# Kernel optimization log

Measured on AMD Instinct MI355X. Metric: run time of the kernel, lower is better.

## Reference

```python
import jax, jax.numpy as jnp
import numpy as np

B, T, D = 2, 4096, 1024
HD, HQ, KVH, W = 128, 8, 1, 1024   # head_dim, q_heads, kv_heads, window
HH, HG, K = 1536, 2048, 4          # hawk hidden, gmlp hidden, conv kernel
ALPHA_SCALE = float(np.log(8.0))   # alpha_log_scale (stored as log, used exp'd)


def setup_inputs() -> dict:
    key = jax.random.key(0)
    ks = jax.random.split(key, 16)
    n = lambda k, shape, std: jax.random.normal(k, shape, jnp.float32) * std
    return {
        'x': n(ks[0], (B, T, D), 1.0),
        'sn_g': jnp.ones((D,), jnp.float32),
        'q_w': n(ks[1], (HQ * HD, D), D ** -0.5),
        'kv_w': n(ks[2], (2 * KVH * HD, D), D ** -0.5),
        'ao_w': n(ks[3], (D, D), D ** -0.5),
        'sgn_g': jnp.ones((D,), jnp.float32),
        'sg_grow': n(ks[4], (2 * HG, D), D ** -0.5),
        'sg_shrink': n(ks[5], (D, HG), HG ** -0.5),
        'hn_g': jnp.ones((D,), jnp.float32),
        'h_in_w': n(ks[6], (2 * HH, D), D ** -0.5),
        'h_conv_w': n(ks[7], (HH, 1, K), K ** -0.5),
        'h_conv_b': jnp.zeros((HH,), jnp.float32),
        'h_gates_w': n(ks[8], (2 * HH, HH), HH ** -0.5),
        'h_gates_b': jnp.zeros((2 * HH,), jnp.float32),
        'h_forget': jnp.linspace(-4.323, -9.0, HH, dtype=jnp.float32),
        'h_out_w': n(ks[9], (D, HH), HH ** -0.5),
        'hgn_g': jnp.ones((D,), jnp.float32),
        'hg_grow': n(ks[10], (2 * HG, D), D ** -0.5),
        'hg_shrink': n(ks[11], (D, HG), HG ** -0.5),
    }


def rmsnorm(x, gamma):
    # original: gamma / dim**-0.5 * x / ||x||_2  (no eps)
    inv = jax.lax.rsqrt(jnp.sum(x * x, axis=-1, keepdims=True))
    return gamma * (x.shape[-1] ** 0.5) * x * inv


def rope(x, base=10000.0):
    # x: (B, T, H, HD); interleaved rotary over time axis 1
    t = x.shape[1]
    hd = x.shape[-1]
    inv = 1.0 / (base ** (jnp.arange(0, hd, 2, dtype=jnp.float32) / hd))
    ang = jnp.arange(t, dtype=jnp.float32)[:, None] * inv[None, :]  # (T, HD/2)
    cos = jnp.cos(ang)[None, :, None, :]
    sin = jnp.sin(ang)[None, :, None, :]
    x1, x2 = x[..., 0::2], x[..., 1::2]
    y1 = x1 * cos - x2 * sin
    y2 = x1 * sin + x2 * cos
    return jnp.stack([y1, y2], axis=-1).reshape(x.shape)


def sliding_mqa(x, q_w, kv_w, ao_w):
    # MQA with causal sliding window of W, computed in blocks of W
    q = (x @ q_w.T).reshape(B, T, HQ, HD)
    kv = (x @ kv_w.T).reshape(B, T, 2, KVH, HD)
    k = kv[:, :, 0, 0]  # (B, T, HD) since KVH == 1
    v = kv[:, :, 1, 0]
    q = rope(q)
    k = rope(k[:, :, None, :])[:, :, 0]
    nb = T // W
    qb = q.reshape(B, nb, W, HQ, HD)
    kb = k.reshape(B, nb, W, HD)
    vb = v.reshape(B, nb, W, HD)
    # prepend previous block (zeros for block 0)
    shift = lambda a: jnp.concatenate([jnp.zeros_like(a[:, :1]), a[:, :-1]], axis=1)
    k2 = jnp.concatenate([shift(kb), kb], axis=2)  # (B, nb, 2W, HD)
    v2 = jnp.concatenate([shift(vb), vb], axis=2)
    qi = jnp.arange(W)[:, None]
    kj = jnp.arange(2 * W)[None, :]
    base = (kj >= qi) & (kj <= qi + W)  # causal + window (i-j <= W)
    blk0 = base & (kj >= W)             # block 0 has no real previous block
    mask = jnp.where(jnp.arange(nb)[:, None, None] == 0, blk0[None], base[None])
    scores = jnp.einsum('bnqhd,bnkd->bhnqk', qb, k2) * (HD ** -0.5)
    scores = jnp.where(mask[None, None], scores, -jnp.inf)
    p = jax.nn.softmax(scores, axis=-1)
    o = jnp.einsum('bhnqk,bnkd->bnqhd', p, v2).reshape(B, T, HQ * HD)
    return o @ ao_w.T


def gated_mlp(x, grow_w, shrink_w):
    gate, h = jnp.split(x @ grow_w.T, 2, axis=-1)
    return (jax.nn.gelu(gate, approximate=False) * h) @ shrink_w.T


def hawk(x, in_w, conv_w, conv_b, gates_w, gates_b, forget_base, out_w):
    gate, u = jnp.split(x @ in_w.T, 2, axis=-1)  # (B, T, HH) each
    # depthwise causal conv1d (torch pads k-1 both sides then slices [:T])
    u_nch = jnp.transpose(u, (0, 2, 1))  # (B, HH, T)
    c = jax.lax.conv_general_dilated(
        u_nch, conv_w, window_strides=(1,), padding=[(K - 1, 0)],
        feature_group_count=HH, dimension_numbers=('NCH', 'OIH', 'NCH'))
    xc = jnp.transpose(c + conv_b[None, :, None], (0, 2, 1))  # (B, T, HH)
    fg, ig = jnp.split(xc @ gates_w.T + gates_b, 2, axis=-1)
    log_alpha = -np.exp(ALPHA_SCALE) * jax.nn.softplus(forget_base) * jax.nn.sigmoid(fg)
    alpha = jnp.exp(log_alpha)
    beta = jnp.sqrt(1.0 - alpha * alpha + 1e-6)
    xin = beta * jax.nn.sigmoid(ig) * xc
    # linear recurrence h_t = alpha_t * h_{t-1} + xin_t  via associative scan
    def combine(c1, c2):
        a1, x1 = c1
        a2, x2 = c2
        return a1 * a2, a2 * x1 + x2
    _, h = jax.lax.associative_scan(combine, (alpha, xin), axis=1)
    return (jax.nn.gelu(gate, approximate=False) * h) @ out_w.T


def reference(x, sn_g, q_w, kv_w, ao_w, sgn_g, sg_grow, sg_shrink,
              hn_g, h_in_w, h_conv_w, h_conv_b, h_gates_w, h_gates_b,
              h_forget, h_out_w, hgn_g, hg_grow, hg_shrink):
    x = x + sliding_mqa(rmsnorm(x, sn_g), q_w, kv_w, ao_w)
    x = x + gated_mlp(rmsnorm(x, sgn_g), sg_grow, sg_shrink)
    x = x + hawk(rmsnorm(x, hn_g), h_in_w, h_conv_w, h_conv_b,
                 h_gates_w, h_gates_b, h_forget, h_out_w)
    x = x + gated_mlp(rmsnorm(x, hgn_g), hg_grow, hg_shrink)
    return x
```

## Files before the change

### kernel.cpp

```cpp
#include <hip/hip_runtime.h>
#include <hip/hip_bf16.h>
#include <math.h>

#define B_  2
#define T_  4096
#define D_  1024
#define HD_ 128
#define HQ_ 8
#define W_  1024
#define HH_ 1536
#define HG_ 2048
#define KC_ 4

typedef float  f32x4  __attribute__((ext_vector_type(4)));
typedef float  f32x2  __attribute__((ext_vector_type(2)));
typedef __bf16 bf16x8 __attribute__((ext_vector_type(8)));
typedef unsigned short u16;
typedef unsigned short u16x2 __attribute__((ext_vector_type(2)));
typedef unsigned short u16x4 __attribute__((ext_vector_type(4)));
typedef unsigned short u16x8 __attribute__((ext_vector_type(8)));

__device__ __forceinline__ u16 f2bf(float f) {
    unsigned int u = __builtin_bit_cast(unsigned int, f);
    u += 0x7fffu + ((u >> 16) & 1u);
    return (u16)(u >> 16);
}
__device__ __forceinline__ float bf2f(u16 v) {
    unsigned int u = ((unsigned int)v) << 16;
    return __builtin_bit_cast(float, u);
}
__device__ __forceinline__ float gelu_exact(float x) {
    return 0.5f * x * (1.0f + erff(x * 0.70710678118654752f));
}
__device__ __forceinline__ float sigmoidf_(float x) {
    return 1.0f / (1.0f + expf(-x));
}

#define GLOAD16(gp, lp) __builtin_amdgcn_global_load_lds( \
    (const __attribute__((address_space(1))) void*)(gp),  \
    (__attribute__((address_space(3))) void*)(lp), 16, 0, 0)

struct CvtArgs {
    const float* src[10];
    u16* dst[10];
    long cum[11];
};
__global__ __launch_bounds__(256)
void cvt_all_kernel(CvtArgs a)
{
    long i = ((long)blockIdx.x * 256 + threadIdx.x) * 8;
    if (i >= a.cum[10]) return;
    int seg = 0;
#pragma unroll
    for (int s = 1; s < 10; s++) if (i >= a.cum[s]) seg = s;
    long off = i - a.cum[seg];
    const float* src = a.src[seg];
    u16* dst = a.dst[seg];
    f32x4 x = *(const f32x4*)(src + off);
    f32x4 y = *(const f32x4*)(src + off + 4);
    u16x4 ua, ub;
    ua.x = f2bf(x.x); ua.y = f2bf(x.y); ua.z = f2bf(x.z); ua.w = f2bf(x.w);
    ub.x = f2bf(y.x); ub.y = f2bf(y.y); ub.z = f2bf(y.z); ub.w = f2bf(y.w);
    *(u16x4*)(dst + off) = ua;
    *(u16x4*)(dst + off + 4) = ub;
}

template<int EPI, bool OBF>
__global__ __launch_bounds__(512)
void gemm_big_kernel(const u16* __restrict__ A, const u16* __restrict__ Bw,
                     const float* __restrict__ bias, const float* __restrict__ res,
                     const u16* gatebuf, void* outv,
                     int M, int N, int K)
{
    __shared__ u16 lA[3][256 * 32];
    __shared__ u16 lB[3][128 * 32];
    const int wg0 = blockIdx.x + gridDim.x * blockIdx.y;
    const int cpx = (gridDim.x * gridDim.y) >> 3;
    const int wgs = (wg0 & 7) * cpx + (wg0 >> 3);
    const int n0 = (wgs % gridDim.x) * 128, m0 = (wgs / gridDim.x) * 256;
    const int tid = threadIdx.x, w = tid >> 6, l = tid & 63;
    const int wr = w >> 1, wc = w & 1;
    const int lr = l & 15, lg = l >> 4;

    f32x4 acc[4][4];
#pragma unroll
    for (int i = 0; i < 4; i++)
#pragma unroll
        for (int j = 0; j < 4; j++) acc[i][j] = {0.f, 0.f, 0.f, 0.f};

    const int srow = tid >> 2;
    const int gslot = (((tid) & 3) - ((tid >> 3) & 3)) & 3;
    const u16* gA = A + (long)(m0 + srow) * K + gslot * 8;
    const u16* gB = Bw + (long)(n0 + srow) * K + gslot * 8;
    const int lofs = tid * 8;

#define STAGE_G(buf, kk)                                            \
    {                                                               \
        GLOAD16(gA + (kk),                 &lA[buf][lofs]);         \
        GLOAD16(gA + (long)128 * K + (kk), &lA[buf][4096 + lofs]);  \
        GLOAD16(gB + (kk),                 &lB[buf][lofs]);         \
    }

    const int NT = K >> 5;
    STAGE_G(0, 0);
    STAGE_G(1, 32);

    const int swzr = (lr >> 1) & 3;
    int cur = 0;
    for (int t = 0; t < NT; ++t) {
        if (t == NT - 1) { asm volatile("s_waitcnt vmcnt(0)" ::: "memory"); }
        else             { asm volatile("s_waitcnt vmcnt(3)" ::: "memory"); }
        __builtin_amdgcn_s_barrier();
        __builtin_amdgcn_sched_barrier(0);
        if (t + 2 < NT) {
            int nb = cur + 2; if (nb >= 3) nb -= 3;
            STAGE_G(nb, (t + 2) << 5);
        }
        bf16x8 af[4], bfr[4];
#pragma unroll
        for (int m = 0; m < 4; m++)
            af[m] = *(const bf16x8*)&lA[cur][(wr * 64 + m * 16 + lr) * 32 + (((lg + swzr) & 3) * 8)];
#pragma unroll
        for (int n = 0; n < 4; n++)
            bfr[n] = *(const bf16x8*)&lB[cur][(wc * 64 + n * 16 + lr) * 32 + (((lg + swzr) & 3) * 8)];
        __builtin_amdgcn_s_setprio(1);
#pragma unroll
        for (int m = 0; m < 4; m++)
#pragma unroll
            for (int n = 0; n < 4; n++)
                acc[m][n] = __builtin_amdgcn_mfma_f32_16x16x32_bf16(af[m], bfr[n], acc[m][n], 0, 0, 0);
        __builtin_amdgcn_s_setprio(0);
        cur++; if (cur == 3) cur = 0;
    }
#undef STAGE_G

#pragma unroll
    for (int m = 0; m < 4; m++)
#pragma unroll
        for (int n = 0; n < 4; n++) {
            const int col = n0 + wc * 64 + n * 16 + lr;
            const float bv = (EPI == 1) ? bias[col] : 0.f;
#pragma unroll
            for (int r = 0; r < 4; r++) {
                const int row = m0 + wr * 64 + m * 16 + lg * 4 + r;
                const long idx = (long)row * N + col;
                float v = acc[m][n][r] + bv;
                if (EPI == 2) v += res[idx];
                if (EPI == 3) v = gelu_exact(bf2f(gatebuf[idx])) * v;
                if (OBF) ((u16*)outv)[idx] = f2bf(v);
                else     ((float*)outv)[idx] = v;
            }
        }
}

template<int EPI, bool OBF>
__global__ __launch_bounds__(256)
void gemm_bf16_kernel(const u16* __restrict__ A, const u16* __restrict__ Bw,
                      const float* __restrict__ bias, const float* __restrict__ res,
                      const u16* gatebuf, void* outv,
                      int M, int N, int K)
{
    __shared__ u16 lA[3][128 * 32];
    __shared__ u16 lB[3][128 * 32];
    const int wg0 = blockIdx.x + gridDim.x * blockIdx.y;
    const int cpx = (gridDim.x * gridDim.y) >> 3;
    const int wgs = (wg0 & 7) * cpx + (wg0 >> 3);
    const int n0 = (wgs % gridDim.x) * 128, m0 = (wgs / gridDim.x) * 128;
    const int tid = threadIdx.x, w = tid >> 6, l = tid & 63;
    const int wr = w >> 1, wc = w & 1, lr = l & 15, lg = l >> 4;

    f32x4 acc[4][4];
#pragma unroll
    for (int i = 0; i < 4; i++)
#pragma unroll
        for (int j = 0; j < 4; j++) acc[i][j] = {0.f, 0.f, 0.f, 0.f};

    const int srow = w * 16 + (l >> 2);
    const int gslot = ((l & 3) - ((l >> 3) & 3)) & 3;
    const u16* gA = A + (long)(m0 + srow) * K + gslot * 8;
    const u16* gB = Bw + (long)(n0 + srow) * K + gslot * 8;
    const int lofs = w * 512 + l * 8;

#define STAGE_G(buf, kk)                                          \
    {                                                             \
        GLOAD16(gA + (kk),                &lA[buf][lofs]);        \
        GLOAD16(gA + (long)64 * K + (kk), &lA[buf][2048 + lofs]); \
        GLOAD16(gB + (kk),                &lB[buf][lofs]);        \
        GLOAD16(gB + (long)64 * K + (kk), &lB[buf][2048 + lofs]); \
    }

    const int NT = K >> 5;
    STAGE_G(0, 0);
    STAGE_G(1, 32);

    const int swzr = (lr >> 1) & 3;
    int cur = 0;
    for (int t = 0; t < NT; ++t) {
        if (t == NT - 1) { asm volatile("s_waitcnt vmcnt(0)" ::: "memory"); }
        else             { asm volatile("s_waitcnt vmcnt(4)" ::: "memory"); }
        __builtin_amdgcn_s_barrier();
        __builtin_amdgcn_sched_barrier(0);
        if (t + 2 < NT) {
            int nb = cur + 2; if (nb >= 3) nb -= 3;
            STAGE_G(nb, (t + 2) << 5);
        }
        bf16x8 af[4], bfr[4];
#pragma unroll
        for (int m = 0; m < 4; m++)
            af[m] = *(const bf16x8*)&lA[cur][(wr * 64 + m * 16 + lr) * 32 + (((lg + swzr) & 3) * 8)];
#pragma unroll
        for (int n = 0; n < 4; n++)
            bfr[n] = *(const bf16x8*)&lB[cur][(wc * 64 + n * 16 + lr) * 32 + (((lg + swzr) & 3) * 8)];
        __builtin_amdgcn_s_setprio(1);
#pragma unroll
        for (int m = 0; m < 4; m++)
#pragma unroll
            for (int n = 0; n < 4; n++)
                acc[m][n] = __builtin_amdgcn_mfma_f32_16x16x32_bf16(af[m], bfr[n], acc[m][n], 0, 0, 0);
        __builtin_amdgcn_s_setprio(0);
        cur++; if (cur == 3) cur = 0;
    }
#undef STAGE_G

#pragma unroll
    for (int m = 0; m < 4; m++)
#pragma unroll
        for (int n = 0; n < 4; n++) {
            const int col = n0 + wc * 64 + n * 16 + lr;
            const float bv = (EPI == 1) ? bias[col] : 0.f;
#pragma unroll
            for (int r = 0; r < 4; r++) {
                const int row = m0 + wr * 64 + m * 16 + lg * 4 + r;
                const long idx = (long)row * N + col;
                float v = acc[m][n][r] + bv;
                if (EPI == 2) v += res[idx];
                if (EPI == 3) v = gelu_exact(bf2f(gatebuf[idx])) * v;
                if (OBF) ((u16*)outv)[idx] = f2bf(v);
                else     ((float*)outv)[idx] = v;
            }
        }
}

__global__ __launch_bounds__(256)
void rmsnorm_kernel(const float* __restrict__ x, const float* __restrict__ g,
                    u16* __restrict__ out)
{
    const long row = blockIdx.x;
    const int tid = threadIdx.x;
    const float* xp = x + row * D_;
    f32x4 v = *(const f32x4*)(xp + tid * 4);
    float ss = v.x * v.x + v.y * v.y + v.z * v.z + v.w * v.w;
#pragma unroll
    for (int o = 1; o < 64; o <<= 1) ss += __shfl_xor(ss, o);
    __shared__ float ps[4];
    if ((tid & 63) == 0) ps[tid >> 6] = ss;
    __syncthreads();
    float tot = ps[0] + ps[1] + ps[2] + ps[3];
    float inv = rsqrtf(tot) * 32.0f;
    f32x4 gv = *(const f32x4*)(g + tid * 4);
    u16x4 o4;
    o4.x = f2bf(gv.x * v.x * inv); o4.y = f2bf(gv.y * v.y * inv);
    o4.z = f2bf(gv.z * v.z * inv); o4.w = f2bf(gv.w * v.w * inv);
    *(u16x4*)(out + row * D_ + tid * 4) = o4;
}

__global__ void rope_bf16_kernel(const float* __restrict__ q, const float* __restrict__ kv,
                                 u16* __restrict__ qb, u16* __restrict__ kb)
{
    const long NQ = (long)B_ * T_ * HQ_ * 64;
    const long NK = (long)B_ * T_ * 64;
    long idx = (long)blockIdx.x * blockDim.x + threadIdx.x;
    if (idx >= NQ + NK) return;
    int i; long t; const float* src; u16* dst;
    if (idx < NQ) {
        i = idx & 63;
        long bth = idx >> 6;
        t = (bth / HQ_) % T_;
        src = q + bth * HD_ + 2 * i;
        dst = qb + bth * HD_ + 2 * i;
    } else {
        long k = idx - NQ;
        i = k & 63;
        long bt = k >> 6;
        t = bt % T_;
        src = kv + bt * (2 * HD_) + 2 * i;
        dst = kb + bt * HD_ + 2 * i;
    }
    float freq = exp2f(-(float)i * 0.20762050593046014f);
    float ang = (float)t * freq;
    float sn, cs;
    sincosf(ang, &sn, &cs);
    f32x2 xv = *(const f32x2*)src;
    u16x2 yv;
    yv.x = f2bf(xv.x * cs - xv.y * sn);
    yv.y = f2bf(xv.x * sn + xv.y * cs);
    *(u16x2*)dst = yv;
}

__global__ __launch_bounds__(256)
void vtrans_kernel(const float* __restrict__ kv, u16* __restrict__ vt)
{
    __shared__ float tile[64][65];
    const int t0 = blockIdx.x * 64, d0 = blockIdx.y * 64, b = blockIdx.z;
    const int tid = threadIdx.x;
    {
        const int tl = tid & 63, dg = tid >> 6;
        const float* vp = kv + (((long)b * T_ + t0 + tl) * 2 + 1) * HD_ + d0 + dg * 16;
#pragma unroll
        for (int j = 0; j < 4; j++) {
            f32x4 v = *(const f32x4*)(vp + j * 4);
            tile[dg * 16 + j * 4 + 0][tl] = v.x;
            tile[dg * 16 + j * 4 + 1][tl] = v.y;
            tile[dg * 16 + j * 4 + 2][tl] = v.z;
            tile[dg * 16 + j * 4 + 3][tl] = v.w;
        }
    }
    __syncthreads();
    {
        const int dl = tid >> 2, tg = (tid & 3) * 16;
        u16x8 a, c;
#pragma unroll
        for (int j = 0; j < 8; j++) a[j] = f2bf(tile[dl][tg + j]);
#pragma unroll
        for (int j = 0; j < 8; j++) c[j] = f2bf(tile[dl][tg + 8 + j]);
        u16* dst = vt + ((long)b * HD_ + d0 + dl) * T_ + t0 + tg;
        *(u16x8*)dst = a;
        *(u16x8*)(dst + 8) = c;
    }
}

#define PLD 72

__global__ __launch_bounds__(256)
void attn_mfma3_kernel(const u16* __restrict__ qb, const u16* __restrict__ kb,
                       const u16* __restrict__ vt, u16* __restrict__ o)
{
    __shared__ u16 Ksh[2][64 * 128];
    __shared__ u16 Vsh[2][128 * 64];
    __shared__ u16 Psh[4 * 16 * PLD];

    const int qt = blockIdx.x, h = blockIdx.y, b = blockIdx.z;
    const int q0 = qt * 64;
    const int tid = threadIdx.x;
    const int w = tid >> 6, l = tid & 63;
    const int lr = l & 15, lg = l >> 4;

    bf16x8 qfr[4];
    {
        const u16* qp = qb + (((long)b * T_ + q0 + w * 16 + lr) * HQ_ + h) * HD_;
#pragma unroll
        for (int kt = 0; kt < 4; kt++)
            qfr[kt] = *(const bf16x8*)(qp + kt * 32 + lg * 8);
    }

    int oK[4], oV[4];
#pragma unroll
    for (int i = 0; i < 4; i++) {
        int krow = w * 16 + i * 4 + (l >> 4);
        int kc8 = (l & 15) ^ (krow & 7);
        oK[i] = krow * 128 + kc8 * 8;
        int vrow = w * 32 + i * 8 + (l >> 3);
        int vc8 = (l & 7) ^ (vrow & 7);
        oV[i] = vrow * T_ + vc8 * 8;
    }
    const u16* kbase = kb + (long)b * T_ * HD_;
    const u16* vbase = vt + (long)b * HD_ * T_;

    f32x4 oacc[8];
#pragma unroll
    for (int dt = 0; dt < 8; dt++) oacc[dt] = {0.f, 0.f, 0.f, 0.f};
    float mrun[4], srun[4];
#pragma unroll
    for (int r = 0; r < 4; r++) { mrun[r] = -1e30f; srun[r] = 0.f; }

    const int kt_lo = (q0 >= W_) ? (q0 - W_) : 0;
    const int nt = ((q0 - kt_lo) >> 6) + 1;
    const int sw = lr & 7;
    const float scale = 0.08838834764831845f;

#pragma unroll
    for (int i = 0; i < 4; i++) {
        GLOAD16(kbase + (long)kt_lo * HD_ + oK[i], &Ksh[0][w * 2048 + i * 512]);
        GLOAD16(vbase + kt_lo + oV[i], &Vsh[0][w * 2048 + i * 512]);
    }

    for (int t = 0; t < nt; ++t) {
        const int kt0 = kt_lo + t * 64;
        const int cur = t & 1;
        if (t + 1 < nt) {
            const int ktn = kt0 + 64;
#pragma unroll
            for (int i = 0; i < 4; i++) {
                GLOAD16(kbase + (long)ktn * HD_ + oK[i], &Ksh[cur ^ 1][w * 2048 + i * 512]);
                GLOAD16(vbase + ktn + oV[i], &Vsh[cur ^ 1][w * 2048 + i * 512]);
            }
            asm volatile("s_waitcnt vmcnt(8)" ::: "memory");
        } else {
            asm volatile("s_waitcnt vmcnt(0)" ::: "memory");
        }
        __builtin_amdgcn_s_barrier();
        __builtin_amdgcn_sched_barrier(0);

        const u16* Kc = Ksh[cur];
        const u16* Vc = Vsh[cur];

        f32x4 s[4];
        __builtin_amdgcn_s_setprio(1);
#pragma unroll
        for (int ct = 0; ct < 4; ct++) {
            s[ct] = {0.f, 0.f, 0.f, 0.f};
#pragma unroll
            for (int kt = 0; kt < 4; kt++) {
                bf16x8 kf = *(const bf16x8*)&Kc[(ct * 16 + lr) * 128 + (((kt * 4 + lg) ^ sw) * 8)];
                s[ct] = __builtin_amdgcn_mfma_f32_16x16x32_bf16(qfr[kt], kf, s[ct], 0, 0, 0);
            }
        }
        __builtin_amdgcn_s_setprio(0);

        float tmax[4] = {-3e38f, -3e38f, -3e38f, -3e38f};
        if (kt0 == q0) {
#pragma unroll
            for (int ct = 0; ct < 4; ct++) {
                const int kpos = kt0 + ct * 16 + lr;
#pragma unroll
                for (int r = 0; r < 4; r++) {
                    const int qpos = q0 + w * 16 + lg * 4 + r;
                    float v = s[ct][r] * scale;
                    v = (kpos <= qpos) ? v : -3e38f;
                    s[ct][r] = v;
                    tmax[r] = fmaxf(tmax[r], v);
                }
            }
        } else if (kt0 == q0 - W_) {
#pragma unroll
            for (int ct = 0; ct < 4; ct++) {
                const int kpos = kt0 + ct * 16 + lr;
#pragma unroll
                for (int r = 0; r < 4; r++) {
                    const int qpos = q0 + w * 16 + lg * 4 + r;
                    float v = s[ct][r] * scale;
                    v = (kpos + W_ >= qpos) ? v : -3e38f;
                    s[ct][r] = v;
                    tmax[r] = fmaxf(tmax[r], v);
                }
            }
        } else {
#pragma unroll
            for (int ct = 0; ct < 4; ct++)
#pragma unroll
                for (int r = 0; r < 4; r++) {
                    float v = s[ct][r] * scale;
                    s[ct][r] = v;
                    tmax[r] = fmaxf(tmax[r], v);
                }
        }
#pragma unroll
        for (int r = 0; r < 4; r++)
#pragma unroll
            for (int msk = 1; msk < 16; msk <<= 1)
                tmax[r] = fmaxf(tmax[r], __shfl_xor(tmax[r], msk));

        bool defer = (tmax[0] <= mrun[0] + 8.f) && (tmax[1] <= mrun[1] + 8.f) &&
                     (tmax[2] <= mrun[2] + 8.f) && (tmax[3] <= mrun[3] + 8.f);
        if (!__all(defer)) {
            float frv[4];
#pragma unroll
            for (int r = 0; r < 4; r++) {
                float mnew = fmaxf(mrun[r], tmax[r]);
                frv[r] = __expf(mrun[r] - mnew);
                mrun[r] = mnew;
                srun[r] *= frv[r];
            }
#pragma unroll
            for (int dt = 0; dt < 8; dt++) {
                oacc[dt][0] *= frv[0]; oacc[dt][1] *= frv[1];
                oacc[dt][2] *= frv[2]; oacc[dt][3] *= frv[3];
            }
        }

        u16* pw = &Psh[w * 16 * PLD];
        float psum[4] = {0.f, 0.f, 0.f, 0.f};
#pragma unroll
        for (int ct = 0; ct < 4; ct++)
#pragma unroll
            for (int r = 0; r < 4; r++) {
                float p = __expf(s[ct][r] - mrun[r]);
                psum[r] += p;
                pw[(lg * 4 + r) * PLD + ct * 16 + lr] = f2bf(p);
            }
#pragma unroll
        for (int r = 0; r < 4; r++) {
#pragma unroll
            for (int msk = 1; msk < 16; msk <<= 1)
                psum[r] += __shfl_xor(psum[r], msk);
            srun[r] += psum[r];
        }

        asm volatile("s_waitcnt lgkmcnt(0)" ::: "memory");
        bf16x8 pa0 = *(const bf16x8*)&pw[lr * PLD + lg * 8];
        bf16x8 pa1 = *(const bf16x8*)&pw[lr * PLD + 32 + lg * 8];
        __builtin_amdgcn_s_setprio(1);
#pragma unroll
        for (int dt = 0; dt < 8; dt++) {
            bf16x8 vf0 = *(const bf16x8*)&Vc[(dt * 16 + lr) * 64 + ((lg ^ sw) * 8)];
            bf16x8 vf1 = *(const bf16x8*)&Vc[(dt * 16 + lr) * 64 + (((4 + lg) ^ sw) * 8)];
            oacc[dt] = __builtin_amdgcn_mfma_f32_16x16x32_bf16(pa0, vf0, oacc[dt], 0, 0, 0);
            oacc[dt] = __builtin_amdgcn_mfma_f32_16x16x32_bf16(pa1, vf1, oacc[dt], 0, 0, 0);
        }
        __builtin_amdgcn_s_setprio(0);
        __syncthreads();
    }

#pragma unroll
    for (int r = 0; r < 4; r++) {
        const int qpos = q0 + w * 16 + lg * 4 + r;
        float inv = 1.f / srun[r];
        u16* op = o + ((long)b * T_ + qpos) * (HQ_ * HD_) + h * HD_;
#pragma unroll
        for (int dt = 0; dt < 8; dt++)
            op[dt * 16 + lr] = f2bf(oacc[dt][r] * inv);
    }
}

__global__ void conv_kernel(const u16* __restrict__ u, const float* __restrict__ w,
                            const float* __restrict__ bias, u16* __restrict__ xc)
{
    long idx = (long)blockIdx.x * blockDim.x + threadIdx.x;
    if (idx >= (long)B_ * T_ * HH_) return;
    int ch = (int)(idx % HH_);
    long row = idx / HH_;
    int t = (int)(row % T_);
    float acc = bias[ch];
#pragma unroll
    for (int k = 0; k < KC_; k++) {
        int ts = t - 3 + k;
        if (ts >= 0) acc += bf2f(u[(row - t + ts) * HH_ + ch]) * w[ch * KC_ + k];
    }
    xc[idx] = f2bf(acc);
}

#define CS_ 64
#define NC_ (T_ / CS_)

__device__ __forceinline__ void alpha_xin(const u16 fg, const u16 ig, const u16 xc,
                                          float sp, float& a, float& xin)
{
    a = expf(-8.0f * sp * sigmoidf_(bf2f(fg)));
    xin = sqrtf(1.f - a * a + 1e-6f) * sigmoidf_(bf2f(ig)) * bf2f(xc);
}

__global__ void scan1_kernel(const u16* __restrict__ fg, const u16* __restrict__ ig,
                             const u16* __restrict__ xc, const float* __restrict__ fb,
                             float* __restrict__ P, float* __restrict__ L)
{
    long idx = (long)blockIdx.x * blockDim.x + threadIdx.x;
    if (idx >= (long)B_ * NC_ * HH_) return;
    int ch = (int)(idx % HH_);
    int chunk = (int)((idx / HH_) % NC_);
    int b = (int)(idx / ((long)HH_ * NC_));
    long base = ((long)b * T_ + chunk * CS_) * HH_ + ch;
    float f = fb[ch];
    float sp = (f > 20.f) ? f : log1pf(expf(f));
    float p = 1.f, lacc = 0.f;
    for (int i = 0; i < CS_; i++) {
        long o = base + (long)i * HH_;
        float a, xin;
        alpha_xin(fg[o], ig[o], xc[o], sp, a, xin);
        lacc = a * lacc + xin;
        p *= a;
    }
    P[idx] = p; L[idx] = lacc;
}
__global__ void scan2_kernel(const float* __restrict__ P, const float* __restrict__ L,
                             float* __restrict__ I)
{
    long idx = (long)blockIdx.x * blockDim.x + threadIdx.x;
    if (idx >= (long)B_ * HH_) return;
    int ch = (int)(idx % HH_);
    int b = (int)(idx / HH_);
    float init = 0.f;
    for (int c = 0; c < NC_; c++) {
        long o = ((long)b * NC_ + c) * HH_ + ch;
        I[o] = init;
        init = P[o] * init + L[o];
    }
}
__global__ void scan3_kernel(const u16* __restrict__ fg, const u16* __restrict__ ig,
                             const u16* __restrict__ xc, const float* __restrict__ fb,
                             const float* __restrict__ I, const u16* __restrict__ gate,
                             u16* __restrict__ glu)
{
    long idx = (long)blockIdx.x * blockDim.x + threadIdx.x;
    if (idx >= (long)B_ * NC_ * HH_) return;
    int ch = (int)(idx % HH_);
    int chunk = (int)((idx / HH_) % NC_);
    int b = (int)(idx / ((long)HH_ * NC_));
    long base = ((long)b * T_ + chunk * CS_) * HH_ + ch;
    float f = fb[ch];
    float sp = (f > 20.f) ? f : log1pf(expf(f));
    float h = I[idx];
    for (int i = 0; i < CS_; i++) {
        long o = base + (long)i * HH_;
        float a, xin;
        alpha_xin(fg[o], ig[o], xc[o], sp, a, xin);
        h = a * h + xin;
        glu[o] = f2bf(gelu_exact(bf2f(gate[o])) * h);
    }
}

static inline long cdivl(long a, long b) { return (a + b - 1) / b; }

extern "C" void kernel_launch(void* const* d_in, const int* in_sizes, int n_in,
                              void* d_out, int out_size, void* d_ws, size_t ws_size,
                              hipStream_t stream)
{
    const float* x_in   = (const float*)d_in[0];
    const float* sn_g   = (const float*)d_in[1];
    const float* q_w    = (const float*)d_in[2];
    const float* kv_w   = (const float*)d_in[3];
    const float* ao_w   = (const float*)d_in[4];
    const float* sgn_g  = (const float*)d_in[5];
    const float* sg_grow   = (const float*)d_in[6];
    const float* sg_shrink = (const float*)d_in[7];
    const float* hn_g   = (const float*)d_in[8];
    const float* h_in_w = (const float*)d_in[9];
    const float* h_conv_w = (const float*)d_in[10];
    const float* h_conv_b = (const float*)d_in[11];
    const float* h_gates_w = (const float*)d_in[12];
    const float* h_gates_b = (const float*)d_in[13];
    const float* h_forget  = (const float*)d_in[14];
    const float* h_out_w   = (const float*)d_in[15];
    const float* hgn_g  = (const float*)d_in[16];
    const float* hg_grow   = (const float*)d_in[17];
    const float* hg_shrink = (const float*)d_in[18];
    float* out = (float*)d_out;

    char* wsb = (char*)d_ws;
    u16* Wq  = (u16*)wsb;
    u16* Wkv = Wq  + 1048576;
    u16* Wao = Wkv + 262144;
    u16* Wsg = Wao + 1048576;
    u16* Wss = Wsg + 4194304;
    u16* Whi = Wss + 2097152;
    u16* Whg = Whi + 3145728;
    u16* Who = Whg + 4718592;
    u16* Wgg = Who + 1572864;
    u16* Wgs = Wgg + 4194304;
    char* ab = wsb + 48758784;
    u16*   XN   = (u16*)(ab + 0);
    char*  S2   = ab + 16777216;
    char*  S3   = ab + 50331648;
    char*  S4   = ab + 75497472;
    char*  S5   = ab + 100663296;
    char*  S6   = ab + 125829120;
    float* PB   = (float*)(ab + 150994944);
    float* LB   = (float*)(ab + 151781376);
    float* IB   = (float*)(ab + 152567808);

    const long M = (long)B_ * T_;
    dim3 blk(256);
    dim3 blk5(512);
    const float* NULF = nullptr;
    const u16*   NULB = nullptr;

    {
        CvtArgs ca;
        const float* srcs[10] = {q_w, kv_w, ao_w, sg_grow, sg_shrink,
                                 h_in_w, h_gates_w, h_out_w, hg_grow, hg_shrink};
        u16* dsts[10] = {Wq, Wkv, Wao, Wsg, Wss, Whi, Whg, Who, Wgg, Wgs};
        long ns[10] = {1048576, 262144, 1048576, 4194304, 2097152,
                       3145728, 4718592, 1572864, 4194304, 2097152};
        long cum = 0;
        for (int i = 0; i < 10; i++) {
            ca.src[i] = srcs[i]; ca.dst[i] = dsts[i]; ca.cum[i] = cum; cum += ns[i];
        }
        ca.cum[10] = cum;
        cvt_all_kernel<<<dim3(cdivl(cum / 8, 256)), blk, 0, stream>>>(ca);
    }

    {
        float* Q  = (float*)S2;
        float* KV = (float*)S3;
        u16*   Kb = (u16*)(S3 + 8388608);
        u16*   Vt = (u16*)(S3 + 10485760);
        u16*   Qb = (u16*)S4;
        u16*   AT = (u16*)S5;
        rmsnorm_kernel<<<dim3(M), blk, 0, stream>>>(x_in, sn_g, XN);
        gemm_bf16_kernel<0,false><<<dim3(8, 64), blk, 0, stream>>>(XN, Wq, NULF, NULF, NULB, Q, M, 1024, 1024);
        gemm_bf16_kernel<0,false><<<dim3(2, 64), blk, 0, stream>>>(XN, Wkv, NULF, NULF, NULB, KV, M, 256, 1024);
        rope_bf16_kernel<<<dim3(cdivl((long)B_ * T_ * (HQ_ + 1) * 64, 256)), blk, 0, stream>>>(Q, KV, Qb, Kb);
        vtrans_kernel<<<dim3(T_ / 64, 2, B_), blk, 0, stream>>>(KV, Vt);
        attn_mfma3_kernel<<<dim3(T_ / 64, HQ_, B_), blk, 0, stream>>>(Qb, Kb, Vt, AT);
        gemm_bf16_kernel<2,false><<<dim3(8, 64), blk, 0, stream>>>(AT, Wao, NULF, x_in, NULB, out, M, 1024, 1024);
    }

    {
        u16* GATE = (u16*)S2;
        rmsnorm_kernel<<<dim3(M), blk, 0, stream>>>(out, sgn_g, XN);
        gemm_big_kernel<0,true><<<dim3(16, 32), blk5, 0, stream>>>(XN, Wsg, NULF, NULF, NULB, GATE, M, 2048, 1024);
        gemm_big_kernel<3,true><<<dim3(16, 32), blk5, 0, stream>>>(XN, Wsg + (size_t)2048 * 1024, NULF, NULF, GATE, GATE, M, 2048, 1024);
        gemm_bf16_kernel<2,false><<<dim3(8, 64), blk, 0, stream>>>(GATE, Wss, NULF, out, NULB, out, M, 1024, 2048);
    }

    {
        u16* GATEH = (u16*)S2;
        u16* U     = (u16*)S3;
        u16* XC    = (u16*)S4;
        u16* FG    = (u16*)S5;
        u16* IG    = (u16*)S6;
        rmsnorm_kernel<<<dim3(M), blk, 0, stream>>>(out, hn_g, XN);
        gemm_bf16_kernel<0,true><<<dim3(12, 64), blk, 0, stream>>>(XN, Whi, NULF, NULF, NULB, GATEH, M, 1536, 1024);
        gemm_bf16_kernel<0,true><<<dim3(12, 64), blk, 0, stream>>>(XN, Whi + (size_t)1536 * 1024, NULF, NULF, NULB, U, M, 1536, 1024);
        conv_kernel<<<dim3(cdivl(M * HH_, 256)), blk, 0, stream>>>(U, h_conv_w, h_conv_b, XC);
        gemm_bf16_kernel<1,true><<<dim3(12, 64), blk, 0, stream>>>(XC, Whg, h_gates_b, NULF, NULB, FG, M, 1536, 1536);
        gemm_bf16_kernel<1,true><<<dim3(12, 64), blk, 0, stream>>>(XC, Whg + (size_t)1536 * 1536, h_gates_b + 1536, NULF, NULB, IG, M, 1536, 1536);
        scan1_kernel<<<dim3(cdivl((long)B_ * NC_ * HH_, 256)), blk, 0, stream>>>(FG, IG, XC, h_forget, PB, LB);
        scan2_kernel<<<dim3(cdivl((long)B_ * HH_, 256)), blk, 0, stream>>>(PB, LB, IB);
        scan3_kernel<<<dim3(cdivl((long)B_ * NC_ * HH_, 256)), blk, 0, stream>>>(FG, IG, XC, h_forget, IB, GATEH, U);
        gemm_bf16_kernel<2,false><<<dim3(8, 64), blk, 0, stream>>>(U, Who, NULF, out, NULB, out, M, 1024, 1536);
    }

    {
        u16* GLU = (u16*)S2;
        rmsnorm_kernel<<<dim3(M), blk, 0, stream>>>(out, hgn_g, XN);
        gemm_big_kernel<0,true><<<dim3(16, 32), blk5, 0, stream>>>(XN, Wgg, NULF, NULF, NULB, GLU, M, 2048, 1024);
        gemm_big_kernel<3,true><<<dim3(16, 32), blk5, 0, stream>>>(XN, Wgg + (size_t)2048 * 1024, NULF, NULF, GLU, GLU, M, 2048, 1024);
        gemm_bf16_kernel<2,false><<<dim3(8, 64), blk, 0, stream>>>(GLU, Wgs, NULF, out, NULB, out, M, 1024, 2048);
    }
}
```

Before: 933.9 us.

## Merge QKV and gate GEMMs, defer softmax row reductions in attention

The Q and KV projections become one GEMM with N=1280, writing an interleaved QKV buffer that rope and the V-transpose kernels now index directly. The two Hawk gate projections likewise become one GEMM with N=3072, which the scan kernels read with a row stride of 3072. In the attention kernel, the cross-lane row-max shuffle now runs only when a rescale is actually needed. The row-sum shuffle is moved out of the loop into a single reduction at the end. The aim is fewer launches, better GEMM utilisation and fewer shuffles per tile, at the cost of a new buffer layout and strided gate reads in the scan.

```diff
diff --git a/kernel.cpp b/kernel.cpp
--- a/kernel.cpp
+++ b/kernel.cpp
@@ -264,7 +264,7 @@
     *(u16x4*)(out + row * D_ + tid * 4) = o4;
 }
 
-__global__ void rope_bf16_kernel(const float* __restrict__ q, const float* __restrict__ kv,
+__global__ void rope_bf16_kernel(const float* __restrict__ qkv,
                                  u16* __restrict__ qb, u16* __restrict__ kb)
 {
     const long NQ = (long)B_ * T_ * HQ_ * 64;
@@ -275,15 +275,17 @@
     if (idx < NQ) {
         i = idx & 63;
         long bth = idx >> 6;
-        t = (bth / HQ_) % T_;
-        src = q + bth * HD_ + 2 * i;
+        long bt = bth >> 3;
+        int h = (int)(bth & 7);
+        t = bt % T_;
+        src = qkv + bt * 1280 + h * HD_ + 2 * i;
         dst = qb + bth * HD_ + 2 * i;
     } else {
         long k = idx - NQ;
         i = k & 63;
         long bt = k >> 6;
         t = bt % T_;
-        src = kv + bt * (2 * HD_) + 2 * i;
+        src = qkv + bt * 1280 + 1024 + 2 * i;
         dst = kb + bt * HD_ + 2 * i;
     }
     float freq = exp2f(-(float)i * 0.20762050593046014f);
@@ -298,14 +300,14 @@
 }
 
 __global__ __launch_bounds__(256)
-void vtrans_kernel(const float* __restrict__ kv, u16* __restrict__ vt)
+void vtrans_kernel(const float* __restrict__ qkv, u16* __restrict__ vt)
 {
     __shared__ float tile[64][65];
     const int t0 = blockIdx.x * 64, d0 = blockIdx.y * 64, b = blockIdx.z;
     const int tid = threadIdx.x;
     {
         const int tl = tid & 63, dg = tid >> 6;
-        const float* vp = kv + (((long)b * T_ + t0 + tl) * 2 + 1) * HD_ + d0 + dg * 16;
+        const float* vp = qkv + (long)((long)b * T_ + t0 + tl) * 1280 + 1152 + d0 + dg * 16;
 #pragma unroll
         for (int j = 0; j < 4; j++) {
             f32x4 v = *(const f32x4*)(vp + j * 4);
@@ -332,7 +334,7 @@
 #define PLD 72
 
 __global__ __launch_bounds__(256)
-void attn_mfma3_kernel(const u16* __restrict__ qb, const u16* __restrict__ kb,
+void attn_mfma6_kernel(const u16* __restrict__ qb, const u16* __restrict__ kb,
                        const u16* __restrict__ vt, u16* __restrict__ o)
 {
     __shared__ u16 Ksh[2][64 * 128];
@@ -417,7 +419,7 @@
         }
         __builtin_amdgcn_s_setprio(0);
 
-        float tmax[4] = {-3e38f, -3e38f, -3e38f, -3e38f};
+        float tm[4] = {-3e38f, -3e38f, -3e38f, -3e38f};
         if (kt0 == q0) {
 #pragma unroll
             for (int ct = 0; ct < 4; ct++) {
@@ -428,7 +430,7 @@
                     float v = s[ct][r] * scale;
                     v = (kpos <= qpos) ? v : -3e38f;
                     s[ct][r] = v;
-                    tmax[r] = fmaxf(tmax[r], v);
+                    tm[r] = fmaxf(tm[r], v);
                 }
             }
         } else if (kt0 == q0 - W_) {
@@ -441,7 +443,7 @@
                     float v = s[ct][r] * scale;
                     v = (kpos + W_ >= qpos) ? v : -3e38f;
                     s[ct][r] = v;
-                    tmax[r] = fmaxf(tmax[r], v);
+                    tm[r] = fmaxf(tm[r], v);
                 }
             }
         } else {
@@ -451,22 +453,22 @@
                 for (int r = 0; r < 4; r++) {
                     float v = s[ct][r] * scale;
                     s[ct][r] = v;
-                    tmax[r] = fmaxf(tmax[r], v);
+                    tm[r] = fmaxf(tm[r], v);
                 }
         }
-#pragma unroll
-        for (int r = 0; r < 4; r++)
-#pragma unroll
-            for (int msk = 1; msk < 16; msk <<= 1)
-                tmax[r] = fmaxf(tmax[r], __shfl_xor(tmax[r], msk));
-
-        bool defer = (tmax[0] <= mrun[0] + 8.f) && (tmax[1] <= mrun[1] + 8.f) &&
-                     (tmax[2] <= mrun[2] + 8.f) && (tmax[3] <= mrun[3] + 8.f);
+
+        bool defer = (tm[0] <= mrun[0] + 8.f) && (tm[1] <= mrun[1] + 8.f) &&
+                     (tm[2] <= mrun[2] + 8.f) && (tm[3] <= mrun[3] + 8.f);
         if (!__all(defer)) {
+#pragma unroll
+            for (int r = 0; r < 4; r++)
+#pragma unroll
+                for (int msk = 1; msk < 16; msk <<= 1)
+                    tm[r] = fmaxf(tm[r], __shfl_xor(tm[r], msk));
             float frv[4];
 #pragma unroll
             for (int r = 0; r < 4; r++) {
-                float mnew = fmaxf(mrun[r], tmax[r]);
+                float mnew = fmaxf(mrun[r], tm[r]);
                 frv[r] = __expf(mrun[r] - mnew);
                 mrun[r] = mnew;
                 srun[r] *= frv[r];
@@ -479,22 +481,14 @@
         }
 
         u16* pw = &Psh[w * 16 * PLD];
-        float psum[4] = {0.f, 0.f, 0.f, 0.f};
 #pragma unroll
         for (int ct = 0; ct < 4; ct++)
 #pragma unroll
             for (int r = 0; r < 4; r++) {
                 float p = __expf(s[ct][r] - mrun[r]);
-                psum[r] += p;
+                srun[r] += p;
                 pw[(lg * 4 + r) * PLD + ct * 16 + lr] = f2bf(p);
             }
-#pragma unroll
-        for (int r = 0; r < 4; r++) {
-#pragma unroll
-            for (int msk = 1; msk < 16; msk <<= 1)
-                psum[r] += __shfl_xor(psum[r], msk);
-            srun[r] += psum[r];
-        }
 
         asm volatile("s_waitcnt lgkmcnt(0)" ::: "memory");
         bf16x8 pa0 = *(const bf16x8*)&pw[lr * PLD + lg * 8];
@@ -510,6 +504,12 @@
         __builtin_amdgcn_s_setprio(0);
         __syncthreads();
     }
+
+#pragma unroll
+    for (int r = 0; r < 4; r++)
+#pragma unroll
+        for (int msk = 1; msk < 16; msk <<= 1)
+            srun[r] += __shfl_xor(srun[r], msk);
 
 #pragma unroll
     for (int r = 0; r < 4; r++) {
@@ -549,7 +549,7 @@
     xin = sqrtf(1.f - a * a + 1e-6f) * sigmoidf_(bf2f(ig)) * bf2f(xc);
 }
 
-__global__ void scan1_kernel(const u16* __restrict__ fg, const u16* __restrict__ ig,
+__global__ void scan1_kernel(const u16* __restrict__ gates,
                              const u16* __restrict__ xc, const float* __restrict__ fb,
                              float* __restrict__ P, float* __restrict__ L)
 {
@@ -558,14 +558,15 @@
     int ch = (int)(idx % HH_);
     int chunk = (int)((idx / HH_) % NC_);
     int b = (int)(idx / ((long)HH_ * NC_));
-    long base = ((long)b * T_ + chunk * CS_) * HH_ + ch;
+    long row0 = (long)b * T_ + chunk * CS_;
     float f = fb[ch];
     float sp = (f > 20.f) ? f : log1pf(expf(f));
     float p = 1.f, lacc = 0.f;
     for (int i = 0; i < CS_; i++) {
-        long o = base + (long)i * HH_;
+        long rg = (row0 + i) * 3072;
+        long rx = (row0 + i) * HH_;
         float a, xin;
-        alpha_xin(fg[o], ig[o], xc[o], sp, a, xin);
+        alpha_xin(gates[rg + ch], gates[rg + 1536 + ch], xc[rx + ch], sp, a, xin);
         lacc = a * lacc + xin;
         p *= a;
     }
@@ -585,7 +586,7 @@
         init = P[o] * init + L[o];
     }
 }
-__global__ void scan3_kernel(const u16* __restrict__ fg, const u16* __restrict__ ig,
+__global__ void scan3_kernel(const u16* __restrict__ gates,
                              const u16* __restrict__ xc, const float* __restrict__ fb,
                              const float* __restrict__ I, const u16* __restrict__ gate,
                              u16* __restrict__ glu)
@@ -595,16 +596,17 @@
     int ch = (int)(idx % HH_);
     int chunk = (int)((idx / HH_) % NC_);
     int b = (int)(idx / ((long)HH_ * NC_));
-    long base = ((long)b * T_ + chunk * CS_) * HH_ + ch;
+    long row0 = (long)b * T_ + chunk * CS_;
     float f = fb[ch];
     float sp = (f > 20.f) ? f : log1pf(expf(f));
     float h = I[idx];
     for (int i = 0; i < CS_; i++) {
-        long o = base + (long)i * HH_;
+        long rg = (row0 + i) * 3072;
+        long rx = (row0 + i) * HH_;
         float a, xin;
-        alpha_xin(fg[o], ig[o], xc[o], sp, a, xin);
+        alpha_xin(gates[rg + ch], gates[rg + 1536 + ch], xc[rx + ch], sp, a, xin);
         h = a * h + xin;
-        glu[o] = f2bf(gelu_exact(bf2f(gate[o])) * h);
+        glu[rx + ch] = f2bf(gelu_exact(bf2f(gate[rx + ch])) * h);
     }
 }
 
@@ -649,10 +651,6 @@
     char* ab = wsb + 48758784;
     u16*   XN   = (u16*)(ab + 0);
     char*  S2   = ab + 16777216;
-    char*  S3   = ab + 50331648;
-    char*  S4   = ab + 75497472;
-    char*  S5   = ab + 100663296;
-    char*  S6   = ab + 125829120;
     float* PB   = (float*)(ab + 150994944);
     float* LB   = (float*)(ab + 151781376);
     float* IB   = (float*)(ab + 152567808);
@@ -679,18 +677,16 @@
     }
 
     {
-        float* Q  = (float*)S2;
-        float* KV = (float*)S3;
-        u16*   Kb = (u16*)(S3 + 8388608);
-        u16*   Vt = (u16*)(S3 + 10485760);
-        u16*   Qb = (u16*)S4;
-        u16*   AT = (u16*)S5;
+        float* QKV = (float*)(ab + 16777216);
+        u16*   Kb  = (u16*)(ab + 58720256);
+        u16*   Vt  = (u16*)(ab + 60817408);
+        u16*   Qb  = (u16*)(ab + 62914560);
+        u16*   AT  = (u16*)(ab + 79691776);
         rmsnorm_kernel<<<dim3(M), blk, 0, stream>>>(x_in, sn_g, XN);
-        gemm_bf16_kernel<0,false><<<dim3(8, 64), blk, 0, stream>>>(XN, Wq, NULF, NULF, NULB, Q, M, 1024, 1024);
-        gemm_bf16_kernel<0,false><<<dim3(2, 64), blk, 0, stream>>>(XN, Wkv, NULF, NULF, NULB, KV, M, 256, 1024);
-        rope_bf16_kernel<<<dim3(cdivl((long)B_ * T_ * (HQ_ + 1) * 64, 256)), blk, 0, stream>>>(Q, KV, Qb, Kb);
-        vtrans_kernel<<<dim3(T_ / 64, 2, B_), blk, 0, stream>>>(KV, Vt);
-        attn_mfma3_kernel<<<dim3(T_ / 64, HQ_, B_), blk, 0, stream>>>(Qb, Kb, Vt, AT);
+        gemm_bf16_kernel<0,false><<<dim3(10, 64), blk, 0, stream>>>(XN, Wq, NULF, NULF, NULB, QKV, M, 1280, 1024);
+        rope_bf16_kernel<<<dim3(cdivl((long)B_ * T_ * (HQ_ + 1) * 64, 256)), blk, 0, stream>>>(QKV, Qb, Kb);
+        vtrans_kernel<<<dim3(T_ / 64, 2, B_), blk, 0, stream>>>(QKV, Vt);
+        attn_mfma6_kernel<<<dim3(T_ / 64, HQ_, B_), blk, 0, stream>>>(Qb, Kb, Vt, AT);
         gemm_bf16_kernel<2,false><<<dim3(8, 64), blk, 0, stream>>>(AT, Wao, NULF, x_in, NULB, out, M, 1024, 1024);
     }
 
@@ -703,20 +699,18 @@
     }
 
     {
-        u16* GATEH = (u16*)S2;
-        u16* U     = (u16*)S3;
-        u16* XC    = (u16*)S4;
-        u16* FG    = (u16*)S5;
-        u16* IG    = (u16*)S6;
+        u16* GATEH = (u16*)(ab + 16777216);
+        u16* U     = (u16*)(ab + 41943040);
+        u16* XC    = (u16*)(ab + 67108864);
+        u16* GATES = (u16*)(ab + 92274688);
         rmsnorm_kernel<<<dim3(M), blk, 0, stream>>>(out, hn_g, XN);
         gemm_bf16_kernel<0,true><<<dim3(12, 64), blk, 0, stream>>>(XN, Whi, NULF, NULF, NULB, GATEH, M, 1536, 1024);
         gemm_bf16_kernel<0,true><<<dim3(12, 64), blk, 0, stream>>>(XN, Whi + (size_t)1536 * 1024, NULF, NULF, NULB, U, M, 1536, 1024);
         conv_kernel<<<dim3(cdivl(M * HH_, 256)), blk, 0, stream>>>(U, h_conv_w, h_conv_b, XC);
-        gemm_bf16_kernel<1,true><<<dim3(12, 64), blk, 0, stream>>>(XC, Whg, h_gates_b, NULF, NULB, FG, M, 1536, 1536);
-        gemm_bf16_kernel<1,true><<<dim3(12, 64), blk, 0, stream>>>(XC, Whg + (size_t)1536 * 1536, h_gates_b + 1536, NULF, NULB, IG, M, 1536, 1536);
-        scan1_kernel<<<dim3(cdivl((long)B_ * NC_ * HH_, 256)), blk, 0, stream>>>(FG, IG, XC, h_forget, PB, LB);
+        gemm_bf16_kernel<1,true><<<dim3(24, 64), blk, 0, stream>>>(XC, Whg, h_gates_b, NULF, NULB, GATES, M, 3072, 1536);
+        scan1_kernel<<<dim3(cdivl((long)B_ * NC_ * HH_, 256)), blk, 0, stream>>>(GATES, XC, h_forget, PB, LB);
         scan2_kernel<<<dim3(cdivl((long)B_ * HH_, 256)), blk, 0, stream>>>(PB, LB, IB);
-        scan3_kernel<<<dim3(cdivl((long)B_ * NC_ * HH_, 256)), blk, 0, stream>>>(FG, IG, XC, h_forget, IB, GATEH, U);
+        scan3_kernel<<<dim3(cdivl((long)B_ * NC_ * HH_, 256)), blk, 0, stream>>>(GATES, XC, h_forget, IB, GATEH, U);
         gemm_bf16_kernel<2,false><<<dim3(8, 64), blk, 0, stream>>>(U, Who, NULF, out, NULB, out, M, 1024, 1536);
     }
 
```

Result: faster. 891.0 us (-4.6%).
